# Performance work log

Hardware: AMD Instinct MI355X
Metric: run time of the kernel (lower is better)

Reference implementation:

```python
import jax, jax.numpy as jnp
import numpy as np


def setup_inputs() -> dict:
    key = jax.random.key(0)
    ks = jax.random.split(key, 12)
    B, T, n, m = 128, 64, 81, 128
    inp = {
        "X": jax.random.normal(ks[0], (B, T, n), dtype=jnp.float32),
        "h0": jax.random.normal(ks[1], (B, m), dtype=jnp.float32),
        "s0": jax.random.normal(ks[2], (B, m), dtype=jnp.float32),
        "W_lstm": jax.random.normal(ks[3], (n, 4 * m), dtype=jnp.float32) * 0.05,
        "U_lstm": jax.random.normal(ks[4], (m, 4 * m), dtype=jnp.float32) * 0.05,
        "b_lstm": jax.random.normal(ks[5], (4 * m,), dtype=jnp.float32) * 0.05,
        "We_w": jax.random.normal(ks[6], (2 * m, T), dtype=jnp.float32) * 0.05,
        "We_b": jax.random.normal(ks[7], (T,), dtype=jnp.float32) * 0.05,
        "Ue_w": jax.random.normal(ks[8], (T, T), dtype=jnp.float32) * 0.05,
        "Ue_b": jax.random.normal(ks[9], (T,), dtype=jnp.float32) * 0.05,
        "ve_w": jax.random.normal(ks[10], (T, 1), dtype=jnp.float32) * 0.05,
        "ve_b": jax.random.normal(ks[11], (1,), dtype=jnp.float32) * 0.05,
    }
    return inp


def reference(X, h0, s0, W_lstm, U_lstm, b_lstm, We_w, We_b, Ue_w, Ue_b, ve_w, ve_b):
    # Faithful to the TF code: initial_state=[h0, s0] is re-passed at every t,
    # so each timestep is an INDEPENDENT single LSTM cell step from (h0, s0).
    # This lets us vectorize the whole Python loop over t.
    B, T, n = X.shape
    m = h0.shape[1]
    # gates for all timesteps at once: (B, T, 4m). Keras gate order: i, f, g(c), o.
    gates = jnp.einsum('btn,ng->btg', X, W_lstm) + (h0 @ U_lstm + b_lstm)[:, None, :]
    i = jax.nn.sigmoid(gates[..., 0 * m:1 * m])
    f = jax.nn.sigmoid(gates[..., 1 * m:2 * m])
    g = jnp.tanh(gates[..., 2 * m:3 * m])
    o = jax.nn.sigmoid(gates[..., 3 * m:4 * m])
    c = f * s0[:, None, :] + i * g          # (B, T, m)
    h = o * jnp.tanh(c)                     # (B, T, m)
    # Input attention, vectorized over t.
    hc = jnp.concatenate([h, c], axis=-1)   # (B, T, 2m)
    A = hc @ We_w + We_b                    # (B, T, T)  = W_e([h;c]) per step t
    U = jnp.einsum('btn,tk->bnk', X, Ue_w) + Ue_b  # (B, n, T) = U_e(X^T)
    # e[b,t,i] = v_e(tanh(A[b,t,:] + U[b,i,:]))
    e = jnp.tanh(A[:, :, None, :] + U[:, None, :, :])       # (B, T, n, T)
    scores = jnp.einsum('btnk,k->btn', e, ve_w[:, 0]) + ve_b[0]  # (B, T, n)
    alpha = jax.nn.softmax(scores, axis=-1)                 # (B, T, n)
    # stack() gives (T, B, 1, n); tf.multiply broadcasts with X (B, T, n) -> (T, B, T, n)
    out = X[None, :, :, :] * jnp.transpose(alpha, (1, 0, 2))[:, :, None, :]
    return out
```

## Files before the change

### kernel.cpp

```cpp
#include <hip/hip_runtime.h>
#include <math.h>

#define BB 128
#define TT_ 64
#define NN 81
#define MM 128
#define GG 512
#define TN 5184
#define TCH 8
#define NBLK2 (BB * (TT_ / TCH))

__device__ __forceinline__ float sigmoidf_(float x) {
    return 1.0f / (1.0f + __expf(-x));
}
__device__ __forceinline__ float fast_tanh(float x) {
    float e = __expf(2.0f * x);
    return 1.0f - 2.0f / (e + 1.0f);
}

__global__ __launch_bounds__(256) void k1_prep(
    const float* __restrict__ X, const float* __restrict__ h0,
    const float* __restrict__ U_lstm, const float* __restrict__ b_lstm,
    const float* __restrict__ Ue_w, const float* __restrict__ Ue_b,
    float* __restrict__ ws_hb, float* __restrict__ ws_U)
{
    __shared__ float h0l[MM];
    __shared__ float Xl[TN];
    int b = blockIdx.x;
    int tid = threadIdx.x;
    if (tid < MM) h0l[tid] = h0[b * MM + tid];
    for (int p = tid; p < TN; p += 256) Xl[p] = X[b * TN + p];
    __syncthreads();

    {
        float a0 = b_lstm[tid], a1 = b_lstm[tid + 256];
        for (int j = 0; j < MM; ++j) {
            float h = h0l[j];
            a0 += h * U_lstm[j * GG + tid];
            a1 += h * U_lstm[j * GG + tid + 256];
        }
        ws_hb[b * GG + tid]       = a0;
        ws_hb[b * GG + tid + 256] = a1;
    }
    for (int p = tid; p < TN; p += 256) {
        int i = p >> 6, k = p & 63;
        float acc = Ue_b[k];
        for (int t = 0; t < TT_; ++t)
            acc += Xl[t * NN + i] * Ue_w[t * TT_ + k];
        ws_U[b * TN + p] = acc;
    }
}

__global__ __launch_bounds__(256) void k2_main(
    const float* __restrict__ X, const float* __restrict__ s0,
    const float* __restrict__ W_lstm,
    const float* __restrict__ We_w, const float* __restrict__ We_b,
    const float* __restrict__ ve_w, const float* __restrict__ ve_b,
    const float* __restrict__ ws_hb, const float* __restrict__ ws_U,
    float* __restrict__ out)
{
    __shared__ alignas(16) float sXct[NN * TCH];
    __shared__ float sHb[GG];
    __shared__ float sGU[5280];
    __shared__ float sHc[TCH * 256];
    __shared__ float sA[TCH * 65];
    __shared__ float sSc[TCH * NN];
    __shared__ float sVe[TT_];

    int blk = blockIdx.x;
    int b  = blk >> 3;
    int tc = blk & 7;
    int t0 = tc * TCH;
    int tid = threadIdx.x;
    float veb = ve_b[0];

    for (int p = tid; p < NN * TCH; p += 256) {
        float v = X[b * TN + t0 * NN + p];
        int tt = p / NN, np = p - tt * NN;
        sXct[np * TCH + tt] = v;
    }
    sHb[tid]       = ws_hb[b * GG + tid];
    sHb[tid + 256] = ws_hb[b * GG + tid + 256];
    if (tid < TT_) sVe[tid] = ve_w[tid];
    __syncthreads();

    float acc0[TCH], acc1[TCH];
    {
        float h0v = sHb[tid], h1v = sHb[tid + 256];
#pragma unroll
        for (int tt = 0; tt < TCH; ++tt) { acc0[tt] = h0v; acc1[tt] = h1v; }
        for (int n = 0; n < NN; ++n) {
            float w0 = W_lstm[n * GG + tid];
            float w1 = W_lstm[n * GG + tid + 256];
            const float4* xr4 = (const float4*)&sXct[n * TCH];
            float4 xa = xr4[0];
            float4 xb = xr4[1];
            acc0[0] += xa.x * w0; acc1[0] += xa.x * w1;
            acc0[1] += xa.y * w0; acc1[1] += xa.y * w1;
            acc0[2] += xa.z * w0; acc1[2] += xa.z * w1;
            acc0[3] += xa.w * w0; acc1[3] += xa.w * w1;
            acc0[4] += xb.x * w0; acc1[4] += xb.x * w1;
            acc0[5] += xb.y * w0; acc1[5] += xb.y * w1;
            acc0[6] += xb.z * w0; acc1[6] += xb.z * w1;
            acc0[7] += xb.w * w0; acc1[7] += xb.w * w1;
        }
    }
#pragma unroll
    for (int tt = 0; tt < TCH; ++tt) {
        sGU[tt * GG + tid]       = acc0[tt];
        sGU[tt * GG + tid + 256] = acc1[tt];
    }
    __syncthreads();

    for (int p = tid; p < TCH * MM; p += 256) {
        int tt = p >> 7, u = p & 127;
        const float* gr = &sGU[tt * GG];
        float gi = sigmoidf_(gr[u]);
        float gf = sigmoidf_(gr[MM + u]);
        float gg = fast_tanh(gr[2 * MM + u]);
        float go = sigmoidf_(gr[3 * MM + u]);
        float c  = gf * s0[b * MM + u] + gi * gg;
        float h  = go * fast_tanh(c);
        sHc[tt * 256 + u]       = h;
        sHc[tt * 256 + 128 + u] = c;
    }
    __syncthreads();

    {
        int k  = tid & 63;
        int th = tid >> 6;
        float a0 = We_b[k], a1 = a0;
        for (int j = 0; j < 256; ++j) {
            float w = We_w[j * TT_ + k];
            a0 += sHc[th * 256 + j]       * w;
            a1 += sHc[(th + 4) * 256 + j] * w;
        }
        sA[th * 65 + k]       = a0;
        sA[(th + 4) * 65 + k] = a1;
    }
    for (int p = tid; p < TN; p += 256) {
        int i = p >> 6, k = p & 63;
        sGU[i * 65 + k] = ws_U[b * TN + p];
    }
    __syncthreads();

    {
        int wv = tid >> 6;
        int l  = tid & 63;
#pragma unroll
        for (int hh = 0; hh < 2; ++hh) {
            int tt = wv + hh * 4;
            const float* Ar = &sA[tt * 65];
#pragma unroll
            for (int pass = 0; pass < 2; ++pass) {
                int i = l + pass * 64;
                if (i < NN) {
                    const float* Ur = &sGU[i * 65];
                    float acc = 0.f;
                    for (int k = 0; k < TT_; ++k)
                        acc += fast_tanh(Ar[k] + Ur[k]) * sVe[k];
                    sSc[tt * NN + i] = acc + veb;
                }
            }
        }
    }
    __syncthreads();

    {
        int wv = tid >> 6;
        int l  = tid & 63;
#pragma unroll
        for (int hh = 0; hh < 2; ++hh) {
            int tt = wv + hh * 4;
            float a  = sSc[tt * NN + l];
            bool v2  = (l + 64 < NN);
            float b2 = v2 ? sSc[tt * NN + l + 64] : -1e30f;
            float mx = fmaxf(a, b2);
            for (int d = 32; d >= 1; d >>= 1) mx = fmaxf(mx, __shfl_xor(mx, d, 64));
            float ea = __expf(a - mx);
            float eb = v2 ? __expf(b2 - mx) : 0.f;
            float s = ea + eb;
            for (int d = 32; d >= 1; d >>= 1) s += __shfl_xor(s, d, 64);
            float inv = 1.f / s;
            sSc[tt * NN + l] = ea * inv;
            if (v2) sSc[tt * NN + l + 64] = eb * inv;
        }
    }
    __syncthreads();

    {
        const float* Xb = &X[b * TN];
        for (int j = tid; j < TN; j += 256) {
            float x = Xb[j];
            int i = j % NN;
#pragma unroll
            for (int tt = 0; tt < TCH; ++tt) {
                out[((size_t)(t0 + tt) * BB + b) * TN + j] = x * sSc[tt * NN + i];
            }
        }
    }
}

extern "C" void kernel_launch(void* const* d_in, const int* in_sizes, int n_in,
                              void* d_out, int out_size, void* d_ws, size_t ws_size,
                              hipStream_t stream) {
    const float* X      = (const float*)d_in[0];
    const float* h0     = (const float*)d_in[1];
    const float* s0     = (const float*)d_in[2];
    const float* W_lstm = (const float*)d_in[3];
    const float* U_lstm = (const float*)d_in[4];
    const float* b_lstm = (const float*)d_in[5];
    const float* We_w   = (const float*)d_in[6];
    const float* We_b   = (const float*)d_in[7];
    const float* Ue_w   = (const float*)d_in[8];
    const float* Ue_b   = (const float*)d_in[9];
    const float* ve_w   = (const float*)d_in[10];
    const float* ve_b   = (const float*)d_in[11];
    float* out = (float*)d_out;

    float* ws    = (float*)d_ws;
    float* ws_hb = ws;
    float* ws_U  = ws + BB * GG;

    k1_prep<<<BB, 256, 0, stream>>>(X, h0, U_lstm, b_lstm, Ue_w, Ue_b, ws_hb, ws_U);
    k2_main<<<NBLK2, 256, 0, stream>>>(X, s0, W_lstm, We_w, We_b, ve_w, ve_b,
                                       ws_hb, ws_U, out);
}
```

Measured before the change: 269.4 us.

## Split prep kernel across four blocks per batch and simplify score tanh

```diff
diff --git a/kernel.cpp b/kernel.cpp
--- a/kernel.cpp
+++ b/kernel.cpp
@@ -9,6 +9,7 @@
 #define TN 5184
 #define TCH 8
 #define NBLK2 (BB * (TT_ / TCH))
+#define SC_ 2.8853900817779268f
 
 __device__ __forceinline__ float sigmoidf_(float x) {
     return 1.0f / (1.0f + __expf(-x));
@@ -24,30 +25,49 @@
     const float* __restrict__ Ue_w, const float* __restrict__ Ue_b,
     float* __restrict__ ws_hb, float* __restrict__ ws_U)
 {
+    __shared__ float Xl[TN];
+    __shared__ float sUe[64 * 16];
     __shared__ float h0l[MM];
-    __shared__ float Xl[TN];
-    int b = blockIdx.x;
+
+    int blk = blockIdx.x;
+    int b = blk >> 2;
+    int q = blk & 3;
     int tid = threadIdx.x;
-    if (tid < MM) h0l[tid] = h0[b * MM + tid];
+
     for (int p = tid; p < TN; p += 256) Xl[p] = X[b * TN + p];
-    __syncthreads();
-
-    {
-        float a0 = b_lstm[tid], a1 = b_lstm[tid + 256];
+    for (int p = tid; p < 1024; p += 256) {
+        int t = p >> 4, kl = p & 15;
+        sUe[p] = Ue_w[t * TT_ + q * 16 + kl];
+    }
+    if (q == 0 && tid < MM) h0l[tid] = h0[b * MM + tid];
+    __syncthreads();
+
+    if (q == 0) {
+        float2 bl = ((const float2*)b_lstm)[tid];
+        float a0 = bl.x, a1 = bl.y;
         for (int j = 0; j < MM; ++j) {
             float h = h0l[j];
-            a0 += h * U_lstm[j * GG + tid];
-            a1 += h * U_lstm[j * GG + tid + 256];
-        }
-        ws_hb[b * GG + tid]       = a0;
-        ws_hb[b * GG + tid + 256] = a1;
-    }
-    for (int p = tid; p < TN; p += 256) {
-        int i = p >> 6, k = p & 63;
-        float acc = Ue_b[k];
-        for (int t = 0; t < TT_; ++t)
-            acc += Xl[t * NN + i] * Ue_w[t * TT_ + k];
-        ws_U[b * TN + p] = acc;
+            float2 w = ((const float2*)&U_lstm[j * GG])[tid];
+            a0 += h * w.x;
+            a1 += h * w.y;
+        }
+        ((float2*)&ws_hb[b * GG])[tid] = make_float2(a0, a1);
+    }
+
+    int kl = tid & 15;
+    int k  = q * 16 + kl;
+    int ir = tid >> 4;
+    float ueb = Ue_b[k];
+#pragma unroll
+    for (int pass = 0; pass < 6; ++pass) {
+        int i = pass * 16 + ir;
+        if (i < NN) {
+            float acc = ueb;
+#pragma unroll 8
+            for (int t = 0; t < TT_; ++t)
+                acc += Xl[t * NN + i] * sUe[t * 16 + kl];
+            ws_U[b * TN + i * 64 + k] = acc;
+        }
     }
 }
 
@@ -60,7 +80,6 @@
     float* __restrict__ out)
 {
     __shared__ alignas(16) float sXct[NN * TCH];
-    __shared__ float sHb[GG];
     __shared__ float sGU[5280];
     __shared__ float sHc[TCH * 256];
     __shared__ float sA[TCH * 65];
@@ -79,36 +98,32 @@
         int tt = p / NN, np = p - tt * NN;
         sXct[np * TCH + tt] = v;
     }
-    sHb[tid]       = ws_hb[b * GG + tid];
-    sHb[tid + 256] = ws_hb[b * GG + tid + 256];
     if (tid < TT_) sVe[tid] = ve_w[tid];
     __syncthreads();
 
     float acc0[TCH], acc1[TCH];
     {
-        float h0v = sHb[tid], h1v = sHb[tid + 256];
-#pragma unroll
-        for (int tt = 0; tt < TCH; ++tt) { acc0[tt] = h0v; acc1[tt] = h1v; }
+        float2 hbv = ((const float2*)&ws_hb[b * GG])[tid];
+#pragma unroll
+        for (int tt = 0; tt < TCH; ++tt) { acc0[tt] = hbv.x; acc1[tt] = hbv.y; }
         for (int n = 0; n < NN; ++n) {
-            float w0 = W_lstm[n * GG + tid];
-            float w1 = W_lstm[n * GG + tid + 256];
+            float2 w = ((const float2*)&W_lstm[n * GG])[tid];
             const float4* xr4 = (const float4*)&sXct[n * TCH];
             float4 xa = xr4[0];
             float4 xb = xr4[1];
-            acc0[0] += xa.x * w0; acc1[0] += xa.x * w1;
-            acc0[1] += xa.y * w0; acc1[1] += xa.y * w1;
-            acc0[2] += xa.z * w0; acc1[2] += xa.z * w1;
-            acc0[3] += xa.w * w0; acc1[3] += xa.w * w1;
-            acc0[4] += xb.x * w0; acc1[4] += xb.x * w1;
-            acc0[5] += xb.y * w0; acc1[5] += xb.y * w1;
-            acc0[6] += xb.z * w0; acc1[6] += xb.z * w1;
-            acc0[7] += xb.w * w0; acc1[7] += xb.w * w1;
+            acc0[0] += xa.x * w.x; acc1[0] += xa.x * w.y;
+            acc0[1] += xa.y * w.x; acc1[1] += xa.y * w.y;
+            acc0[2] += xa.z * w.x; acc1[2] += xa.z * w.y;
+            acc0[3] += xa.w * w.x; acc1[3] += xa.w * w.y;
+            acc0[4] += xb.x * w.x; acc1[4] += xb.x * w.y;
+            acc0[5] += xb.y * w.x; acc1[5] += xb.y * w.y;
+            acc0[6] += xb.z * w.x; acc1[6] += xb.z * w.y;
+            acc0[7] += xb.w * w.x; acc1[7] += xb.w * w.y;
         }
     }
 #pragma unroll
     for (int tt = 0; tt < TCH; ++tt) {
-        sGU[tt * GG + tid]       = acc0[tt];
-        sGU[tt * GG + tid + 256] = acc1[tt];
+        ((float2*)&sGU[tt * GG])[tid] = make_float2(acc0[tt], acc1[tt]);
     }
     __syncthreads();
 
@@ -135,18 +150,20 @@
             a0 += sHc[th * 256 + j]       * w;
             a1 += sHc[(th + 4) * 256 + j] * w;
         }
-        sA[th * 65 + k]       = a0;
-        sA[(th + 4) * 65 + k] = a1;
+        sA[th * 65 + k]       = a0 * SC_;
+        sA[(th + 4) * 65 + k] = a1 * SC_;
     }
     for (int p = tid; p < TN; p += 256) {
         int i = p >> 6, k = p & 63;
-        sGU[i * 65 + k] = ws_U[b * TN + p];
+        sGU[i * 65 + k] = ws_U[b * TN + p] * SC_;
     }
     __syncthreads();
 
     {
         int wv = tid >> 6;
         int l  = tid & 63;
+        float sumVe = 0.f;
+        for (int k = 0; k < TT_; ++k) sumVe += sVe[k];
 #pragma unroll
         for (int hh = 0; hh < 2; ++hh) {
             int tt = wv + hh * 4;
@@ -157,9 +174,14 @@
                 if (i < NN) {
                     const float* Ur = &sGU[i * 65];
                     float acc = 0.f;
-                    for (int k = 0; k < TT_; ++k)
-                        acc += fast_tanh(Ar[k] + Ur[k]) * sVe[k];
-                    sSc[tt * NN + i] = acc + veb;
+#pragma unroll 8
+                    for (int k = 0; k < TT_; ++k) {
+                        float s = Ar[k] + Ur[k];
+                        float e = exp2f(s);
+                        float r = __builtin_amdgcn_rcpf(e + 1.0f);
+                        acc = fmaf(sVe[k], r, acc);
+                    }
+                    sSc[tt * NN + i] = sumVe - 2.0f * acc + veb;
                 }
             }
         }
@@ -222,7 +244,7 @@
     float* ws_hb = ws;
     float* ws_U  = ws + BB * GG;
 
-    k1_prep<<<BB, 256, 0, stream>>>(X, h0, U_lstm, b_lstm, Ue_w, Ue_b, ws_hb, ws_U);
+    k1_prep<<<BB * 4, 256, 0, stream>>>(X, h0, U_lstm, b_lstm, Ue_w, Ue_b, ws_hb, ws_U);
     k2_main<<<NBLK2, 256, 0, stream>>>(X, s0, W_lstm, We_w, We_b, ve_w, ve_b,
                                        ws_hb, ws_U, out);
 }
```

After: 250.4 us. 1.08x faster.
